# Performance work log

Measured on AMD Instinct MI355X. Metric: run time of the kernel, lower is better.

Reference implementation:

```python
import jax, jax.numpy as jnp
import numpy as np

R = 80   # volume_reso
B, NV, C, H, W = 1, 4, 32, 64, 64


def _voxel_grid():
    line = np.linspace(-1.0, 1.0, R)
    x, y, z = np.meshgrid(line, line, line, indexing='ij')
    return jnp.asarray(np.stack([x, y, z]).reshape(3, -1), dtype=jnp.float32)  # (3, R^3)


def grid_sample_pix(img, coords):
    """Bilinear sample at pixel coords (align_corners=True convention, zero padding).
    img: (BN, C, H, W); coords: (BN, N, 2) as (x, y) in pixel units.
    Returns vals (BN, C, N) and in-bounds mask (BN, N)."""
    BN, Cc, Hh, Ww = img.shape
    x, y = coords[..., 0], coords[..., 1]
    mask = ((x >= 0) & (x <= Ww - 1) & (y >= 0) & (y <= Hh - 1)).astype(img.dtype)
    x0 = jnp.floor(x); y0 = jnp.floor(y)
    x1 = x0 + 1.0;     y1 = y0 + 1.0
    wx1 = x - x0; wx0 = 1.0 - wx1
    wy1 = y - y0; wy0 = 1.0 - wy1
    imgf = img.reshape(BN, Cc, Hh * Ww)

    def corner(xi, yi, w):
        valid = ((xi >= 0) & (xi <= Ww - 1) & (yi >= 0) & (yi <= Hh - 1)).astype(img.dtype)
        xc = jnp.clip(xi, 0, Ww - 1).astype(jnp.int32)
        yc = jnp.clip(yi, 0, Hh - 1).astype(jnp.int32)
        flat = yc * Ww + xc                                   # (BN, N)
        vals = jnp.take_along_axis(imgf, flat[:, None, :], axis=2)  # (BN, C, N)
        return vals * (valid * w)[:, None, :]

    out = (corner(x0, y0, wx0 * wy0) + corner(x1, y0, wx1 * wy0)
           + corner(x0, y1, wx0 * wy1) + corner(x1, y1, wx1 * wy1))
    return out, mask


def setup_inputs() -> dict:
    key = jax.random.key(0)
    ks = jax.random.split(key, 7)
    feats = jax.random.normal(ks[0], (B, NV, C, H, W), dtype=jnp.float32)
    # structured pinhole projection matrices (K @ w2c embedded in 4x4)
    f = 55.0; cx = (W - 1) / 2.0; cy = (H - 1) / 2.0
    poses = np.zeros((B, NV, 4, 4), np.float32)
    for v in range(NV):
        poses[0, v] = np.array([[f, 0, cx, 0.0],
                                [0, f, cy, 0.1 * v],
                                [0, 0, 1.0, 3.0 + 0.2 * v],
                                [0, 0, 0, 1.0]], np.float32)
    return {
        'feats': feats,
        'source_poses': jnp.asarray(poses),
        'W1': jax.random.normal(ks[1], (32, 32), jnp.float32) / np.sqrt(32.0),
        'b1': jax.random.normal(ks[2], (32,), jnp.float32) * 0.01,
        'W2': jax.random.normal(ks[3], (32, 16), jnp.float32) / np.sqrt(32.0),
        'b2': jax.random.normal(ks[4], (16,), jnp.float32) * 0.01,
        'W3': jax.random.normal(ks[5], (16, 8), jnp.float32) / np.sqrt(16.0),
        'b3': jax.random.normal(ks[6], (8,), jnp.float32) * 0.01,
    }


def reference(feats, source_poses, W1, b1, W2, b2, W3, b3):
    N = R ** 3
    xyz = _voxel_grid()                                             # (3, N)
    homo = jnp.concatenate([xyz, jnp.ones((1, N), xyz.dtype)], 0)   # (4, N)
    proj = jnp.einsum('bvij,jn->bvin', source_poses, homo)[:, :, :3]  # (B,NV,3,N)
    z = proj[:, :, 2]                                               # (B,NV,N)
    mask_valid_depth = (z > 0).astype(feats.dtype)
    uv = proj[:, :, :2] / proj[:, :, 2:3]                           # (B,NV,2,N)
    coords = jnp.transpose(uv, (0, 1, 3, 2)).reshape(B * NV, N, 2)
    vals, mask = grid_sample_pix(feats.reshape(B * NV, C, H, W), coords)
    vf = jnp.transpose(vals.reshape(B, NV, C, N), (0, 1, 3, 2))     # (B,NV,N,C)
    mask = mask.reshape(B, NV, N) * mask_valid_depth                # (B,NV,N)
    weight = mask / (jnp.sum(mask, axis=1, keepdims=True) + 1e-8)
    # small MLP 32 -> 32 -> 16 -> 8
    h = jax.nn.relu(vf @ W1 + b1)
    h = jax.nn.relu(h @ W2 + b2)
    h = h @ W3 + b3                                                 # (B,NV,N,8)
    w = weight[..., None]
    mean = jnp.sum(h * w, axis=1, keepdims=True)                    # (B,1,N,8)
    var = jnp.sum(w * (h - mean) ** 2, axis=1)                      # (B,N,8)
    mv = jnp.concatenate([mean[:, 0], var], axis=-1)                # (B,N,16)
    vol = mv.reshape(B, R, R, R, 16)                                # (B,X,Y,Z,16)
    return jnp.transpose(vol, (0, 4, 3, 2, 1))                      # (B,16,Z,Y,X)
```

## Files before the change

kernel.cpp:

```cpp
#include <hip/hip_runtime.h>
#include <cstddef>

#define RR 80
#define NVIEW 4
#define CH 32
#define IH 64
#define IW 64
#define NPIX (IH*IW)
#define NVOX (RR*RR*RR)

#define PLANE_H (NPIX*8)
#define VIEW_H  (4*PLANE_H)

typedef _Float16 half2_t  __attribute__((ext_vector_type(2)));
typedef _Float16 half4_t  __attribute__((ext_vector_type(4)));
typedef _Float16 half8_t  __attribute__((ext_vector_type(8)));
typedef float    float4_t __attribute__((ext_vector_type(4)));

union i2h2 { int i; half2_t h; };

__global__ __launch_bounds__(256) void g_precompute(
    const float* __restrict__ feats, const float* __restrict__ W1,
    _Float16* __restrict__ G)
{
    int g = blockIdx.x >> 6;
    int p = (blockIdx.x & 63)*256 + threadIdx.x;
    __shared__ float sW1[CH*8];
    if (threadIdx.x < CH*8) {
        int ic = threadIdx.x >> 3, e = threadIdx.x & 7;
        sW1[threadIdx.x] = W1[ic*CH + 8*g + e];
    }
    __syncthreads();
    int v  = p >> 12;
    int yx = p & 4095;
    const float* fb = feats + ((size_t)v*CH)*NPIX + yx;
    float acc[8];
    #pragma unroll
    for (int e=0;e<8;++e) acc[e] = 0.f;
    #pragma unroll
    for (int ic=0; ic<CH; ++ic) {
        float fv = fb[(size_t)ic*NPIX];
        #pragma unroll
        for (int e=0;e<8;++e) acc[e] = fmaf(fv, sW1[ic*8+e], acc[e]);
    }
    half8_t h;
    #pragma unroll
    for (int e=0;e<8;++e) h[e] = (_Float16)acc[e];
    *(half8_t*)(G + (size_t)v*VIEW_H + (size_t)g*PLANE_H + (size_t)yx*8) = h;
}

__global__ __launch_bounds__(256) void dgfv_main(
    const _Float16* __restrict__ G,
    const float* __restrict__ poses,
    const float* __restrict__ b1,
    const float* __restrict__ W2, const float* __restrict__ b2,
    const float* __restrict__ W3, const float* __restrict__ b3,
    float* __restrict__ out)
{
    const int wid  = threadIdx.x >> 6;
    const int lane = threadIdx.x & 63;
    const int lq   = lane >> 4;
    const int lc   = lane & 15;
    const int vown  = blockIdx.x*256 + wid*64 + lane;
    const int vbase = blockIdx.x*256 + wid*64 + lc;

    half8_t w2a;
    #pragma unroll
    for (int j=0;j<8;++j) w2a[j] = (_Float16)W2[(lq*8+j)*16 + lc];
    half4_t w3a;
    #pragma unroll
    for (int j=0;j<4;++j) w3a[j] = (_Float16)W3[(lq*4+j)*8 + (lc&7)];
    float4_t c1init, c2init;
    #pragma unroll
    for (int r=0;r<4;++r) {
        c1init[r] = b2[lq*4+r];
        c2init[r] = b3[(lq*4+r)&7];
    }
    half8_t b1h;
    #pragma unroll
    for (int j=0;j<8;++j) b1h[j] = (_Float16)b1[8*lq+j];

    const float step = 2.0f/(float)(RR-1);
    int i  = vown % RR;
    int t  = vown / RR;
    int j_ = t % RR;
    int k_ = t / RR;
    float x = fmaf((float)i,  step, -1.0f);
    float y = fmaf((float)j_, step, -1.0f);
    float z = fmaf((float)k_, step, -1.0f);

    int wpa[NVIEW];
    int wpb[NVIEW];
    int adm[NVIEW];
    #pragma unroll
    for (int v=0; v<NVIEW; ++v) {
        const float* P = poses + v*16;
        float px = fmaf(P[0],x, fmaf(P[1],y, fmaf(P[2], z, P[3])));
        float py = fmaf(P[4],x, fmaf(P[5],y, fmaf(P[6], z, P[7])));
        float pz = fmaf(P[8],x, fmaf(P[9],y, fmaf(P[10],z, P[11])));
        float r0 = __builtin_amdgcn_rcpf(pz);
        r0 = r0*(2.0f - pz*r0);
        float u  = px*r0;
        float w  = py*r0;

        bool ok = (pz > 0.f) && (u >= 0.f) && (u <= (float)(IW-1))
                             && (w >= 0.f) && (w <= (float)(IH-1));

        float uc = fminf(fmaxf(u, 0.f), (float)(IW-1));
        float wc = fminf(fmaxf(w, 0.f), (float)(IH-1));
        float fx0 = floorf(uc), fy0 = floorf(wc);
        float tx = uc - fx0, ty = wc - fy0;
        int x0 = (int)fx0, y0 = (int)fy0;
        float wx0 = 1.f - tx, wy0 = 1.f - ty;

        i2h2 pa, pb;
        pa.h.x = (_Float16)(wx0*wy0);  pa.h.y = (_Float16)(tx*wy0);
        pb.h.x = (_Float16)(wx0*ty);   pb.h.y = (_Float16)(tx*ty);
        wpa[v] = pa.i;
        wpb[v] = pb.i;
        adm[v] = (int)(((unsigned)((y0*IW + x0)*8)) | (ok ? 0x80000000u : 0u));
    }

    const _Float16* Gq = G + (size_t)lq*PLANE_H;

    #pragma unroll
    for (int p=0; p<4; ++p) {
        const int vx   = vbase + 16*p;
        const int srcb = (lc + 16*p) << 2;

        int ra[NVIEW], rb[NVIEW], rm[NVIEW];
        #pragma unroll
        for (int v=0; v<NVIEW; ++v) {
            ra[v] = __builtin_amdgcn_ds_bpermute(srcb, wpa[v]);
            rb[v] = __builtin_amdgcn_ds_bpermute(srcb, wpb[v]);
            rm[v] = __builtin_amdgcn_ds_bpermute(srcb, adm[v]);
        }

        float accA[4], accB[4], accM = 0.f;
        #pragma unroll
        for (int r=0;r<4;++r) { accA[r]=0.f; accB[r]=0.f; }

        #pragma unroll
        for (int v=0; v<NVIEW; ++v) {
            i2h2 ua, ub;  ua.i = ra[v];  ub.i = rb[v];
            const bool ok = (rm[v] < 0);
            const int addr = rm[v] & 0x7FFFFFFF;

            const _Float16* base = Gq + (size_t)v*VIEW_H + addr;
            half8_t a = *(const half8_t*)(base);
            half8_t b = *(const half8_t*)(base + 8);
            half8_t c = *(const half8_t*)(base + IW*8);
            half8_t d = *(const half8_t*)(base + IW*8 + 8);
            half8_t h1 = a*ua.h.x + b*ua.h.y + c*ub.h.x + d*ub.h.y + b1h;
            h1 = __builtin_elementwise_max(h1, (half8_t)(_Float16)0.f);

            float4_t d1 = __builtin_amdgcn_mfma_f32_16x16x32_f16(w2a, h1, c1init, 0,0,0);
            half4_t h2;
            #pragma unroll
            for (int r=0;r<4;++r) h2[r] = (_Float16)fmaxf(d1[r], 0.f);

            float4_t d2 = __builtin_amdgcn_mfma_f32_16x16x16f16(w3a, h2, c2init, 0,0,0);

            #pragma unroll
            for (int r=0;r<4;++r) {
                float h3 = d2[r];
                float hm = ok ? h3 : 0.f;
                accA[r] += hm;
                accB[r]  = fmaf(hm, h3, accB[r]);
            }
            accM += ok ? 1.f : 0.f;
        }

        float S   = accM + 1e-8f;
        float inv = 1.f/S;
        float sw  = accM*inv;
        #pragma unroll
        for (int r=0;r<4;++r) {
            float mean = accA[r]*inv;
            float var  = fmaf(-mean*mean, (2.f - sw), accB[r]*inv);
            float val  = (lq < 2) ? mean : var;
            int   cch  = 4*lq + r;
            out[(size_t)cch*NVOX + vx] = val;
        }
    }
}

extern "C" void kernel_launch(void* const* d_in, const int* in_sizes, int n_in,
                              void* d_out, int out_size, void* d_ws, size_t ws_size,
                              hipStream_t stream)
{
    const float* feats = (const float*)d_in[0];
    const float* poses = (const float*)d_in[1];
    const float* W1    = (const float*)d_in[2];
    const float* b1    = (const float*)d_in[3];
    const float* W2    = (const float*)d_in[4];
    const float* b2    = (const float*)d_in[5];
    const float* W3    = (const float*)d_in[6];
    const float* b3    = (const float*)d_in[7];
    float* out = (float*)d_out;

    _Float16* G = (_Float16*)d_ws;
    g_precompute<<<256, 256, 0, stream>>>(feats, W1, G);
    dgfv_main<<<NVOX/256, 256, 0, stream>>>(G, poses, b1, W2, b2, W3, b3, out);
}
```

Baseline: 99.47 us.

## Interleave per-pixel hidden features, fold b1 into precompute, software-pipeline gathers

The precomputed first-layer features move from four planes of 8 channels into a per-pixel layout of 32 fp16 values, so the four lane groups serving one voxel read one contiguous 64-byte span per corner. The b1 bias is added once during precompute instead of per sample, which is valid because the clamped bilinear weights sum to one. Invalid views now gather from address 0 to keep those loads cache-friendly. The per-view loop becomes explicitly interleaved gather/compute macros so the loads for the next view are in flight while the current view's MFMAs run, at the cost of more live registers.

```diff
diff --git a/kernel.cpp b/kernel.cpp
--- a/kernel.cpp
+++ b/kernel.cpp
@@ -9,8 +9,8 @@
 #define NPIX (IH*IW)
 #define NVOX (RR*RR*RR)
 
-#define PLANE_H (NPIX*8)
-#define VIEW_H  (4*PLANE_H)
+#define PIX_H   32
+#define VIEW_H  (NPIX*PIX_H)
 
 typedef _Float16 half2_t  __attribute__((ext_vector_type(2)));
 typedef _Float16 half4_t  __attribute__((ext_vector_type(4)));
@@ -21,38 +21,39 @@
 
 __global__ __launch_bounds__(256) void g_precompute(
     const float* __restrict__ feats, const float* __restrict__ W1,
-    _Float16* __restrict__ G)
+    const float* __restrict__ b1, _Float16* __restrict__ G)
 {
-    int g = blockIdx.x >> 6;
-    int p = (blockIdx.x & 63)*256 + threadIdx.x;
-    __shared__ float sW1[CH*8];
-    if (threadIdx.x < CH*8) {
-        int ic = threadIdx.x >> 3, e = threadIdx.x & 7;
-        sW1[threadIdx.x] = W1[ic*CH + 8*g + e];
-    }
+    int tid = blockIdx.x*256 + threadIdx.x;
+    int p   = tid >> 1;
+    int hg  = tid & 1;
+    __shared__ float sW1[CH*CH];
+    __shared__ float sb1[CH];
+    for (int t = threadIdx.x; t < CH*CH; t += 256) sW1[t] = W1[t];
+    if (threadIdx.x < CH) sb1[threadIdx.x] = b1[threadIdx.x];
     __syncthreads();
     int v  = p >> 12;
     int yx = p & 4095;
     const float* fb = feats + ((size_t)v*CH)*NPIX + yx;
-    float acc[8];
-    #pragma unroll
-    for (int e=0;e<8;++e) acc[e] = 0.f;
+    float acc[16];
+    #pragma unroll
+    for (int e=0;e<16;++e) acc[e] = sb1[hg*16+e];
     #pragma unroll
     for (int ic=0; ic<CH; ++ic) {
         float fv = fb[(size_t)ic*NPIX];
         #pragma unroll
-        for (int e=0;e<8;++e) acc[e] = fmaf(fv, sW1[ic*8+e], acc[e]);
-    }
-    half8_t h;
-    #pragma unroll
-    for (int e=0;e<8;++e) h[e] = (_Float16)acc[e];
-    *(half8_t*)(G + (size_t)v*VIEW_H + (size_t)g*PLANE_H + (size_t)yx*8) = h;
+        for (int e=0;e<16;++e) acc[e] = fmaf(fv, sW1[ic*CH + hg*16 + e], acc[e]);
+    }
+    half8_t o0, o1;
+    #pragma unroll
+    for (int e=0;e<8;++e) { o0[e] = (_Float16)acc[e]; o1[e] = (_Float16)acc[8+e]; }
+    _Float16* dst = G + (size_t)p*PIX_H + (size_t)hg*16;
+    *(half8_t*)(dst)   = o0;
+    *(half8_t*)(dst+8) = o1;
 }
 
 __global__ __launch_bounds__(256) void dgfv_main(
     const _Float16* __restrict__ G,
     const float* __restrict__ poses,
-    const float* __restrict__ b1,
     const float* __restrict__ W2, const float* __restrict__ b2,
     const float* __restrict__ W3, const float* __restrict__ b3,
     float* __restrict__ out)
@@ -76,9 +77,6 @@
         c1init[r] = b2[lq*4+r];
         c2init[r] = b3[(lq*4+r)&7];
     }
-    half8_t b1h;
-    #pragma unroll
-    for (int j=0;j<8;++j) b1h[j] = (_Float16)b1[8*lq+j];
 
     const float step = 2.0f/(float)(RR-1);
     int i  = vown % RR;
@@ -118,58 +116,71 @@
         pb.h.x = (_Float16)(wx0*ty);   pb.h.y = (_Float16)(tx*ty);
         wpa[v] = pa.i;
         wpb[v] = pb.i;
-        adm[v] = (int)(((unsigned)((y0*IW + x0)*8)) | (ok ? 0x80000000u : 0u));
-    }
-
-    const _Float16* Gq = G + (size_t)lq*PLANE_H;
+        unsigned paddr = (unsigned)((y0*IW + x0)*PIX_H);
+        adm[v] = ok ? (int)(paddr | 0x80000000u) : 0;
+    }
+
+    const _Float16* Gq = G + (size_t)lq*8;
+
+#define GATHER(vv, Av, Bv, Cv, Dv)                                         \
+    do {                                                                   \
+        const _Float16* _bp = Gq + (size_t)(vv)*VIEW_H                     \
+                                 + (size_t)(rm[vv] & 0x7FFFFFFF);          \
+        Av = *(const half8_t*)(_bp);                                       \
+        Bv = *(const half8_t*)(_bp + PIX_H);                       \
+        Cv = *(const half8_t*)(_bp + IW*PIX_H);                    \
+        Dv = *(const half8_t*)(_bp + IW*PIX_H + PIX_H);                    \
+    } while (0)
+
+#define COMPUTE(vv, Av, Bv, Cv, Dv)                                        \
+    do {                                                                   \
+        i2h2 _ua, _ub; _ua.i = ra[vv]; _ub.i = rb[vv];                     \
+        half8_t _h1 = Av*_ua.h.x + Bv*_ua.h.y + Cv*_ub.h.x + Dv*_ub.h.y;   \
+        _h1 = __builtin_elementwise_max(_h1, (half8_t)(_Float16)0.f);      \
+        float4_t _d1 = __builtin_amdgcn_mfma_f32_16x16x32_f16(w2a, _h1, c1init, 0,0,0); \
+        half4_t _h2;                                                       \
+        _h2[0] = (_Float16)fmaxf(_d1[0], 0.f);                             \
+        _h2[1] = (_Float16)fmaxf(_d1[1], 0.f);                             \
+        _h2[2] = (_Float16)fmaxf(_d1[2], 0.f);                             \
+        _h2[3] = (_Float16)fmaxf(_d1[3], 0.f);                             \
+        float4_t _d2 = __builtin_amdgcn_mfma_f32_16x16x16f16(w3a, _h2, c2init, 0,0,0); \
+        const bool _ok = (rm[vv] < 0);                                     \
+        _Pragma("unroll")                                                  \
+        for (int _r=0;_r<4;++_r) {                                         \
+            float _h3 = _d2[_r];                                           \
+            float _hm = _ok ? _h3 : 0.f;                                   \
+            accA[_r] += _hm;                                               \
+            accB[_r]  = fmaf(_hm, _h3, accB[_r]);                          \
+        }                                                                  \
+        accM += _ok ? 1.f : 0.f;                                           \
+    } while (0)
 
     #pragma unroll
     for (int p=0; p<4; ++p) {
         const int vx   = vbase + 16*p;
         const int srcb = (lc + 16*p) << 2;
 
-        int ra[NVIEW], rb[NVIEW], rm[NVIEW];
-        #pragma unroll
-        for (int v=0; v<NVIEW; ++v) {
-            ra[v] = __builtin_amdgcn_ds_bpermute(srcb, wpa[v]);
-            rb[v] = __builtin_amdgcn_ds_bpermute(srcb, wpb[v]);
-            rm[v] = __builtin_amdgcn_ds_bpermute(srcb, adm[v]);
-        }
+        int rm[NVIEW], ra[NVIEW], rb[NVIEW];
+        #pragma unroll
+        for (int v=0; v<NVIEW; ++v) rm[v] = __builtin_amdgcn_ds_bpermute(srcb, adm[v]);
+        #pragma unroll
+        for (int v=0; v<NVIEW; ++v) ra[v] = __builtin_amdgcn_ds_bpermute(srcb, wpa[v]);
+        #pragma unroll
+        for (int v=0; v<NVIEW; ++v) rb[v] = __builtin_amdgcn_ds_bpermute(srcb, wpb[v]);
 
         float accA[4], accB[4], accM = 0.f;
         #pragma unroll
         for (int r=0;r<4;++r) { accA[r]=0.f; accB[r]=0.f; }
 
-        #pragma unroll
-        for (int v=0; v<NVIEW; ++v) {
-            i2h2 ua, ub;  ua.i = ra[v];  ub.i = rb[v];
-            const bool ok = (rm[v] < 0);
-            const int addr = rm[v] & 0x7FFFFFFF;
-
-            const _Float16* base = Gq + (size_t)v*VIEW_H + addr;
-            half8_t a = *(const half8_t*)(base);
-            half8_t b = *(const half8_t*)(base + 8);
-            half8_t c = *(const half8_t*)(base + IW*8);
-            half8_t d = *(const half8_t*)(base + IW*8 + 8);
-            half8_t h1 = a*ua.h.x + b*ua.h.y + c*ub.h.x + d*ub.h.y + b1h;
-            h1 = __builtin_elementwise_max(h1, (half8_t)(_Float16)0.f);
-
-            float4_t d1 = __builtin_amdgcn_mfma_f32_16x16x32_f16(w2a, h1, c1init, 0,0,0);
-            half4_t h2;
-            #pragma unroll
-            for (int r=0;r<4;++r) h2[r] = (_Float16)fmaxf(d1[r], 0.f);
-
-            float4_t d2 = __builtin_amdgcn_mfma_f32_16x16x16f16(w3a, h2, c2init, 0,0,0);
-
-            #pragma unroll
-            for (int r=0;r<4;++r) {
-                float h3 = d2[r];
-                float hm = ok ? h3 : 0.f;
-                accA[r] += hm;
-                accB[r]  = fmaf(hm, h3, accB[r]);
-            }
-            accM += ok ? 1.f : 0.f;
-        }
+        half8_t A0,B0,C0,D0, A1,B1,C1,D1, A2,B2,C2,D2, A3,B3,C3,D3;
+        GATHER(0, A0,B0,C0,D0);
+        GATHER(1, A1,B1,C1,D1);
+        COMPUTE(0, A0,B0,C0,D0);
+        GATHER(2, A2,B2,C2,D2);
+        COMPUTE(1, A1,B1,C1,D1);
+        GATHER(3, A3,B3,C3,D3);
+        COMPUTE(2, A2,B2,C2,D2);
+        COMPUTE(3, A3,B3,C3,D3);
 
         float S   = accM + 1e-8f;
         float inv = 1.f/S;
@@ -183,6 +194,8 @@
             out[(size_t)cch*NVOX + vx] = val;
         }
     }
+#undef GATHER
+#undef COMPUTE
 }
 
 extern "C" void kernel_launch(void* const* d_in, const int* in_sizes, int n_in,
@@ -200,6 +213,6 @@
     float* out = (float*)d_out;
 
     _Float16* G = (_Float16*)d_ws;
-    g_precompute<<<256, 256, 0, stream>>>(feats, W1, G);
-    dgfv_main<<<NVOX/256, 256, 0, stream>>>(G, poses, b1, W2, b2, W3, b3, out);
+    g_precompute<<<128, 256, 0, stream>>>(feats, W1, b1, G);
+    dgfv_main<<<NVOX/256, 256, 0, stream>>>(G, poses, W2, b2, W3, b3, out);
 }
```

New measurement: 101.3 us. No clear change (+1.9%).

## Interleave precomputed features per pixel and fold first-layer bias into precompute

Applied to the files above, without the earlier changes.

The precomputed first-layer activations G change from four 8-channel planes per view to one contiguous 32-half record per pixel. The four lane quads that split the channels now read adjacent 16-byte pieces of the same 64-byte pixel record instead of four far-apart planes, which should give fewer, more coalesced memory transactions per bilinear corner. The b1 bias moves into the precompute, which relies on bilinear weights summing to one for in-bounds samples. Out-of-bounds samples now point at address 0 so masked lanes hit a shared cached line, and the bpermute order is regrouped.

```diff
diff --git a/kernel.cpp b/kernel.cpp
--- a/kernel.cpp
+++ b/kernel.cpp
@@ -9,8 +9,8 @@
 #define NPIX (IH*IW)
 #define NVOX (RR*RR*RR)
 
-#define PLANE_H (NPIX*8)
-#define VIEW_H  (4*PLANE_H)
+#define PIX_H   32
+#define VIEW_H  (NPIX*PIX_H)
 
 typedef _Float16 half2_t  __attribute__((ext_vector_type(2)));
 typedef _Float16 half4_t  __attribute__((ext_vector_type(4)));
@@ -21,38 +21,37 @@
 
 __global__ __launch_bounds__(256) void g_precompute(
     const float* __restrict__ feats, const float* __restrict__ W1,
-    _Float16* __restrict__ G)
+    const float* __restrict__ b1, _Float16* __restrict__ G)
 {
-    int g = blockIdx.x >> 6;
-    int p = (blockIdx.x & 63)*256 + threadIdx.x;
-    __shared__ float sW1[CH*8];
-    if (threadIdx.x < CH*8) {
-        int ic = threadIdx.x >> 3, e = threadIdx.x & 7;
-        sW1[threadIdx.x] = W1[ic*CH + 8*g + e];
-    }
+    int tid = blockIdx.x*256 + threadIdx.x;
+    int p   = tid >> 2;
+    int g   = tid & 3;
+    __shared__ float sW1[CH*CH];
+    __shared__ float sb1[CH];
+    for (int t = threadIdx.x; t < CH*CH; t += 256) sW1[t] = W1[t];
+    if (threadIdx.x < CH) sb1[threadIdx.x] = b1[threadIdx.x];
     __syncthreads();
     int v  = p >> 12;
     int yx = p & 4095;
     const float* fb = feats + ((size_t)v*CH)*NPIX + yx;
     float acc[8];
     #pragma unroll
-    for (int e=0;e<8;++e) acc[e] = 0.f;
+    for (int e=0;e<8;++e) acc[e] = sb1[8*g+e];
     #pragma unroll
     for (int ic=0; ic<CH; ++ic) {
         float fv = fb[(size_t)ic*NPIX];
         #pragma unroll
-        for (int e=0;e<8;++e) acc[e] = fmaf(fv, sW1[ic*8+e], acc[e]);
+        for (int e=0;e<8;++e) acc[e] = fmaf(fv, sW1[ic*CH + 8*g + e], acc[e]);
     }
     half8_t h;
     #pragma unroll
     for (int e=0;e<8;++e) h[e] = (_Float16)acc[e];
-    *(half8_t*)(G + (size_t)v*VIEW_H + (size_t)g*PLANE_H + (size_t)yx*8) = h;
+    *(half8_t*)(G + (size_t)p*PIX_H + (size_t)g*8) = h;
 }
 
 __global__ __launch_bounds__(256) void dgfv_main(
     const _Float16* __restrict__ G,
     const float* __restrict__ poses,
-    const float* __restrict__ b1,
     const float* __restrict__ W2, const float* __restrict__ b2,
     const float* __restrict__ W3, const float* __restrict__ b3,
     float* __restrict__ out)
@@ -76,9 +75,6 @@
         c1init[r] = b2[lq*4+r];
         c2init[r] = b3[(lq*4+r)&7];
     }
-    half8_t b1h;
-    #pragma unroll
-    for (int j=0;j<8;++j) b1h[j] = (_Float16)b1[8*lq+j];
 
     const float step = 2.0f/(float)(RR-1);
     int i  = vown % RR;
@@ -118,23 +114,24 @@
         pb.h.x = (_Float16)(wx0*ty);   pb.h.y = (_Float16)(tx*ty);
         wpa[v] = pa.i;
         wpb[v] = pb.i;
-        adm[v] = (int)(((unsigned)((y0*IW + x0)*8)) | (ok ? 0x80000000u : 0u));
-    }
-
-    const _Float16* Gq = G + (size_t)lq*PLANE_H;
+        unsigned paddr = (unsigned)((y0*IW + x0)*PIX_H);
+        adm[v] = ok ? (int)(paddr | 0x80000000u) : 0;
+    }
+
+    const _Float16* Gq = G + (size_t)lq*8;
 
     #pragma unroll
     for (int p=0; p<4; ++p) {
         const int vx   = vbase + 16*p;
         const int srcb = (lc + 16*p) << 2;
 
-        int ra[NVIEW], rb[NVIEW], rm[NVIEW];
-        #pragma unroll
-        for (int v=0; v<NVIEW; ++v) {
-            ra[v] = __builtin_amdgcn_ds_bpermute(srcb, wpa[v]);
-            rb[v] = __builtin_amdgcn_ds_bpermute(srcb, wpb[v]);
-            rm[v] = __builtin_amdgcn_ds_bpermute(srcb, adm[v]);
-        }
+        int rm[NVIEW], ra[NVIEW], rb[NVIEW];
+        #pragma unroll
+        for (int v=0; v<NVIEW; ++v) rm[v] = __builtin_amdgcn_ds_bpermute(srcb, adm[v]);
+        #pragma unroll
+        for (int v=0; v<NVIEW; ++v) ra[v] = __builtin_amdgcn_ds_bpermute(srcb, wpa[v]);
+        #pragma unroll
+        for (int v=0; v<NVIEW; ++v) rb[v] = __builtin_amdgcn_ds_bpermute(srcb, wpb[v]);
 
         float accA[4], accB[4], accM = 0.f;
         #pragma unroll
@@ -148,10 +145,10 @@
 
             const _Float16* base = Gq + (size_t)v*VIEW_H + addr;
             half8_t a = *(const half8_t*)(base);
-            half8_t b = *(const half8_t*)(base + 8);
-            half8_t c = *(const half8_t*)(base + IW*8);
-            half8_t d = *(const half8_t*)(base + IW*8 + 8);
-            half8_t h1 = a*ua.h.x + b*ua.h.y + c*ub.h.x + d*ub.h.y + b1h;
+            half8_t b = *(const half8_t*)(base + PIX_H);
+            half8_t c = *(const half8_t*)(base + IW*PIX_H);
+            half8_t d = *(const half8_t*)(base + IW*PIX_H + PIX_H);
+            half8_t h1 = a*ua.h.x + b*ua.h.y + c*ub.h.x + d*ub.h.y;
             h1 = __builtin_elementwise_max(h1, (half8_t)(_Float16)0.f);
 
             float4_t d1 = __builtin_amdgcn_mfma_f32_16x16x32_f16(w2a, h1, c1init, 0,0,0);
@@ -200,6 +197,6 @@
     float* out = (float*)d_out;
 
     _Float16* G = (_Float16*)d_ws;
-    g_precompute<<<256, 256, 0, stream>>>(feats, W1, G);
-    dgfv_main<<<NVOX/256, 256, 0, stream>>>(G, poses, b1, W2, b2, W3, b3, out);
+    g_precompute<<<256, 256, 0, stream>>>(feats, W1, b1, G);
+    dgfv_main<<<NVOX/256, 256, 0, stream>>>(G, poses, W2, b2, W3, b3, out);
 }
```

New measurement: 100.5 us. Within noise of the previous version (+1.1%).
